# Optimization experiments

Measured on AMD Instinct MI355X. Metric: run time of the kernel, lower is better.

Reference implementation:

```python
import jax, jax.numpy as jnp
from jax import lax
import numpy as np


def setup_inputs() -> dict:
    key = jax.random.key(0)
    k1, k2, k3 = jax.random.split(key, 3)
    B, H, W, C = 8, 128, 128, 128
    F, KS = 128, 3
    x = jax.random.normal(k1, (B, H, W, C), dtype=jnp.float32)
    style = jax.random.normal(k2, (B, C), dtype=jnp.float32)
    kernel = jax.random.normal(k3, (KS, KS, C, F), dtype=jnp.float32) * 0.05
    return {"x": x, "style": style, "kernel": kernel}


def reference(x, style, kernel):
    """StyleGAN2 modulated+demodulated conv via grouped conv (groups=batch).
    x: (B,H,W,C) NHWC, style: (B,C), kernel: (kh,kw,C,F)."""
    B, H, W, C = x.shape
    kh, kw, Cin, F = kernel.shape
    # Modulate: per-sample scale of input channels -> (B, kh, kw, C, F)
    w = kernel[None] * (style[:, None, None, :, None] + 1.0)
    # Demodulate: normalize each output filter over (kh, kw, Cin)
    w = w / jnp.sqrt(jnp.sum(jnp.square(w), axis=(1, 2, 3), keepdims=True) + 1e-8)
    # Grouped conv trick: fold batch into channels, groups = B
    xg = jnp.transpose(x, (0, 3, 1, 2)).reshape(1, B * C, H, W)   # (1, B*C, H, W)
    wg = jnp.transpose(w, (1, 2, 3, 0, 4)).reshape(kh, kw, Cin, B * F)  # HWIO
    y = lax.conv_general_dilated(
        xg, wg, window_strides=(1, 1), padding="SAME",
        dimension_numbers=("NCHW", "HWIO", "NCHW"),
        feature_group_count=B,
    )  # (1, B*F, H, W)
    y = y.reshape(B, F, H, W)
    return jnp.transpose(y, (0, 2, 3, 1))  # NHWC
```

## Files before the change

### kernel.cpp

```cpp
#include <hip/hip_runtime.h>

typedef __attribute__((ext_vector_type(8))) short short8;
typedef __attribute__((ext_vector_type(8))) unsigned short ushort8;
typedef __attribute__((ext_vector_type(4))) float f32x4;

static __device__ __forceinline__ unsigned short f2bf(float f) {
    union { float f; unsigned int u; } a; a.f = f;
    unsigned int u = a.u;
    return (unsigned short)((u + 0x7fffu + ((u >> 16) & 1u)) >> 16);
}

static __device__ __forceinline__ void gll16(const unsigned short* g, unsigned short* l) {
    __builtin_amdgcn_global_load_lds(
        (const __attribute__((address_space(1))) unsigned int*)g,
        (__attribute__((address_space(3))) unsigned int*)l, 16, 0, 0);
}

#define PROW 16640
#define PPLANE 2163200

__global__ void prep1(const float* __restrict__ x,
                      const float* __restrict__ kern,
                      const float* __restrict__ style,
                      float* __restrict__ partial,
                      unsigned short* __restrict__ xbf) {
    const int t = threadIdx.x;
    if (blockIdx.x < 72) {
        const int rs = blockIdx.x % 9;
        const int b  = blockIdx.x / 9;
        __shared__ float sty[128];
        __shared__ float red[256];
        if (t < 128) sty[t] = style[b * 128 + t] + 1.0f;
        __syncthreads();
        const int f = t & 127, half = t >> 7;
        const float* kp = kern + (size_t)rs * 16384 + f;
        float s = 0.0f;
        #pragma unroll 8
        for (int c = half * 64; c < half * 64 + 64; ++c) {
            float w = kp[(size_t)c * 128] * sty[c];
            s += w * w;
        }
        red[t] = s;
        __syncthreads();
        if (t < 128) partial[((size_t)b * 9 + rs) * 128 + t] = red[t] + red[t + 128];
    } else {
        const int id = (blockIdx.x - 72) * 256 + t;
        if (id >= 8 * 130 * 130 * 16) return;
        const int cg = id & 15;
        const int p  = id >> 4;
        const int wp = p % 130;
        const int q  = p / 130;
        const int hp = q % 130;
        const int b  = q / 130;
        ushort8 v = {0, 0, 0, 0, 0, 0, 0, 0};
        if (hp >= 1 && hp <= 128 && wp >= 1 && wp <= 128) {
            const float4* src = (const float4*)(x + (((size_t)b * 128 + (hp - 1)) * 128 + (wp - 1)) * 128 + cg * 8);
            float4 f0 = src[0];
            float4 f1 = src[1];
            v[0] = f2bf(f0.x); v[1] = f2bf(f0.y); v[2] = f2bf(f0.z); v[3] = f2bf(f0.w);
            v[4] = f2bf(f1.x); v[5] = f2bf(f1.y); v[6] = f2bf(f1.z); v[7] = f2bf(f1.w);
        }
        *(ushort8*)(xbf + (size_t)p * 128 + cg * 8) = v;
    }
}

__global__ void prep_wt(const float* __restrict__ kern,
                        const float* __restrict__ style,
                        const float* __restrict__ partial,
                        unsigned short* __restrict__ wt) {
    const int rs = blockIdx.x, b = blockIdx.y;
    const int t  = threadIdx.x;
    __shared__ float sty[128], dm[128];
    __shared__ float ts[32][132];
    if (t < 128) {
        sty[t] = style[b * 128 + t] + 1.0f;
    } else {
        const int f = t - 128;
        float s = 0.0f;
        #pragma unroll
        for (int r = 0; r < 9; ++r) s += partial[((size_t)b * 9 + r) * 128 + f];
        dm[f] = rsqrtf(s + 1e-8f);
    }
    __syncthreads();
    const float* kp = kern + (size_t)rs * 16384;
    unsigned short* wp = wt + ((size_t)b * 9 + rs) * 16384;
    for (int c0 = 0; c0 < 128; c0 += 32) {
        {
            const int fi = (t & 31) * 4;
            const int ci = t >> 5;
            #pragma unroll
            for (int k = 0; k < 4; ++k) {
                const float4 v = *(const float4*)(kp + (size_t)(c0 + ci + 8 * k) * 128 + fi);
                ts[ci + 8 * k][fi + 0] = v.x;
                ts[ci + 8 * k][fi + 1] = v.y;
                ts[ci + 8 * k][fi + 2] = v.z;
                ts[ci + 8 * k][fi + 3] = v.w;
            }
        }
        __syncthreads();
        {
            const int cb = (t & 7) * 4;
            const int f2 = t >> 3;
            #pragma unroll
            for (int k = 0; k < 4; ++k) {
                const int f = f2 + 32 * k;
                ushort4 o;
                o.x = f2bf(ts[cb + 0][f] * sty[c0 + cb + 0] * dm[f]);
                o.y = f2bf(ts[cb + 1][f] * sty[c0 + cb + 1] * dm[f]);
                o.z = f2bf(ts[cb + 2][f] * sty[c0 + cb + 2] * dm[f]);
                o.w = f2bf(ts[cb + 3][f] * sty[c0 + cb + 3] * dm[f]);
                *(ushort4*)(wp + (size_t)f * 128 + c0 + cb) = o;
            }
        }
        __syncthreads();
    }
}

__global__ __launch_bounds__(512, 4) void mdconv7(const unsigned short* __restrict__ xbf,
                                                  const unsigned short* __restrict__ wt,
                                                  float* __restrict__ out) {
    const int lin = blockIdx.x;
    const int b   = lin & 7;
    const int h2  = (lin >> 3) * 2;
    const int tid = threadIdx.x;

    __shared__ unsigned short lsh[2 * 12288];

    const unsigned short* xb  = xbf + (size_t)b * PPLANE;
    const unsigned short* wtb = wt + (size_t)b * 9 * 16384;

    const int so = (tid & 127) * 128 + (tid >> 7) * 8;

    const int lane = tid & 63;
    const int wv   = tid >> 6;
    const int hw   = wv >> 2;
    const int ww   = (wv >> 1) & 1;
    const int fw   = wv & 1;
    const int fl   = lane & 15;
    const int quad = lane >> 4;

    const int ard = hw * 4096 + quad * 1024 + (ww * 64 + fl) * 8;
    const int brd = 8192 + quad * 1024 + (fw * 64 + fl) * 8;

    f32x4 acc[4][4];
    #pragma unroll
    for (int mt = 0; mt < 4; ++mt)
        #pragma unroll
        for (int ft = 0; ft < 4; ++ft)
            acc[mt][ft] = (f32x4){0.f, 0.f, 0.f, 0.f};

#define STAGE(st, nxt) {                                                          \
    const int rs_ = (st) >> 2, kc_ = (st) & 3;                                    \
    const int r_ = rs_ / 3, s_ = rs_ % 3;                                         \
    const unsigned short* ga0 = xb + ((size_t)(h2 + r_) * 130 + s_) * 128 + kc_ * 32; \
    const unsigned short* gb  = wtb + rs_ * 16384 + kc_ * 32;                     \
    unsigned short* la = lsh + (nxt) * 12288;                                     \
    gll16(ga0 + so,        la + tid * 8);                                         \
    gll16(ga0 + PROW + so, la + 4096 + tid * 8);                                  \
    gll16(gb + so,         la + 8192 + tid * 8);                                  \
}

    STAGE(0, 0);
    __syncthreads();

    #pragma unroll
    for (int st = 0; st < 36; ++st) {
        const int cur = st & 1;
        if (st < 35) STAGE(st + 1, cur ^ 1);
        const int ce = cur * 12288;
        short8 bv[4];
        #pragma unroll
        for (int ft = 0; ft < 4; ++ft)
            bv[ft] = *(const short8*)(lsh + ce + brd + ft * 128);
        #pragma unroll
        for (int mt = 0; mt < 4; ++mt) {
            const short8 av = *(const short8*)(lsh + ce + ard + mt * 128);
            #pragma unroll
            for (int ft = 0; ft < 4; ++ft)
                acc[mt][ft] = __builtin_amdgcn_mfma_f32_16x16x32_bf16(av, bv[ft], acc[mt][ft], 0, 0, 0);
        }
        __syncthreads();
    }
#undef STAGE

    float* ob = out + ((size_t)(b * 128 + h2 + hw) * 128) * 128;
    #pragma unroll
    for (int mt = 0; mt < 4; ++mt) {
        #pragma unroll
        for (int reg = 0; reg < 4; ++reg) {
            const int w = ww * 64 + mt * 16 + quad * 4 + reg;
            #pragma unroll
            for (int ft = 0; ft < 4; ++ft)
                ob[(size_t)w * 128 + fw * 64 + ft * 16 + fl] = acc[mt][ft][reg];
        }
    }
}

__global__ void prep_sumsq(const float* __restrict__ kern,
                           const float* __restrict__ style,
                           float* __restrict__ partial) {
    const int rs = blockIdx.x;
    const int b  = blockIdx.y;
    const int t  = threadIdx.x;
    __shared__ float sty[128];
    __shared__ float red[256];
    if (t < 128) sty[t] = style[b * 128 + t] + 1.0f;
    __syncthreads();
    const int f = t & 127, half = t >> 7;
    const float* kp = kern + (size_t)rs * 16384 + f;
    float s = 0.0f;
    #pragma unroll 8
    for (int c = half * 64; c < half * 64 + 64; ++c) {
        float w = kp[(size_t)c * 128] * sty[c];
        s += w * w;
    }
    red[t] = s;
    __syncthreads();
    if (t < 128) partial[((size_t)b * 9 + rs) * 128 + t] = red[t] + red[t + 128];
}

__global__ void mdconv_fb(const float* __restrict__ x,
                          const unsigned short* __restrict__ wt,
                          float* __restrict__ out) {
    const int lin = blockIdx.x;
    const int b   = lin & 7;
    const int sp  = lin >> 3;
    const int h0  = (sp >> 3) * 8;
    const int w0  = (sp & 7) * 16;
    const int tid = threadIdx.x;
    __shared__ unsigned short xs[180 * 138];
    {
        const float* xb = x + (size_t)b * (128 * 128 * 128);
        for (int id = tid; id < 180 * 16; id += 256) {
            int p  = id >> 4;
            int cg = id & 15;
            int pr = p / 18;
            int pc = p - pr * 18;
            int hh = h0 - 1 + pr;
            int ww = w0 - 1 + pc;
            ushort8 v = {0, 0, 0, 0, 0, 0, 0, 0};
            if ((unsigned)hh < 128u && (unsigned)ww < 128u) {
                const float4* src = (const float4*)(xb + ((size_t)(hh * 128 + ww) * 128 + cg * 8));
                float4 f0 = src[0];
                float4 f1 = src[1];
                v[0] = f2bf(f0.x); v[1] = f2bf(f0.y); v[2] = f2bf(f0.z); v[3] = f2bf(f0.w);
                v[4] = f2bf(f1.x); v[5] = f2bf(f1.y); v[6] = f2bf(f1.z); v[7] = f2bf(f1.w);
            }
            *(ushort8*)(xs + p * 138 + cg * 8) = v;
        }
    }
    __syncthreads();
    const int lane = tid & 63;
    const int wave = tid >> 6;
    const int fl   = lane & 15;
    const int quad = lane >> 4;
    const int kq   = quad * 8;
    f32x4 acc[8][2];
    #pragma unroll
    for (int mt = 0; mt < 8; ++mt)
        #pragma unroll
        for (int j = 0; j < 2; ++j)
            acc[mt][j] = (f32x4){0.f, 0.f, 0.f, 0.f};
    const unsigned short* wtb = wt + (size_t)b * (9 * 128 * 128) + (size_t)wave * 4096 + fl * 128 + kq;
    #pragma unroll
    for (int rs = 0; rs < 9; ++rs) {
        const int r = rs / 3, s = rs % 3;
        #pragma unroll
        for (int kc = 0; kc < 4; ++kc) {
            const int k0 = kc * 32 + kq;
            short8 a[8];
            #pragma unroll
            for (int mt = 0; mt < 8; ++mt)
                a[mt] = *(const short8*)(xs + ((mt + r) * 18 + fl + s) * 138 + k0);
            #pragma unroll
            for (int j = 0; j < 2; ++j) {
                short8 bf = *(const short8*)(wtb + rs * 16384 + j * 2048 + kc * 32);
                #pragma unroll
                for (int mt = 0; mt < 8; ++mt)
                    acc[mt][j] = __builtin_amdgcn_mfma_f32_16x16x32_bf16(a[mt], bf, acc[mt][j], 0, 0, 0);
            }
        }
    }
    float* ob = out + ((size_t)(b * 128 + h0) * 128 + w0) * 128;
    #pragma unroll
    for (int mt = 0; mt < 8; ++mt)
        #pragma unroll
        for (int j = 0; j < 2; ++j) {
            const int f = (wave * 2 + j) * 16 + fl;
            #pragma unroll
            for (int reg = 0; reg < 4; ++reg)
                ob[((size_t)(mt * 128 + quad * 4 + reg)) * 128 + f] = acc[mt][j][reg];
        }
}

extern "C" void kernel_launch(void* const* d_in, const int* in_sizes, int n_in,
                              void* d_out, int out_size, void* d_ws, size_t ws_size,
                              hipStream_t stream) {
    const float* x     = (const float*)d_in[0];
    const float* style = (const float*)d_in[1];
    const float* kern  = (const float*)d_in[2];
    float* out = (float*)d_out;

    const size_t XBF_BYTES = (size_t)8 * 130 * 130 * 128 * 2;
    const size_t WT_BYTES  = (size_t)8 * 9 * 128 * 128 * 2;
    const size_t NEED      = XBF_BYTES + WT_BYTES + 36864;

    if (ws_size >= NEED) {
        unsigned short* xbf = (unsigned short*)d_ws;
        unsigned short* wt  = (unsigned short*)((char*)d_ws + XBF_BYTES);
        float* partial      = (float*)((char*)d_ws + XBF_BYTES + WT_BYTES);
        prep1<<<dim3(72 + 8450), dim3(256), 0, stream>>>(x, kern, style, partial, xbf);
        prep_wt<<<dim3(9, 8), dim3(256), 0, stream>>>(kern, style, partial, wt);
        mdconv7<<<dim3(512), dim3(512), 0, stream>>>(xbf, wt, out);
    } else {
        unsigned short* wt = (unsigned short*)d_ws;
        float* partial     = (float*)((char*)d_ws + WT_BYTES);
        prep_sumsq<<<dim3(9, 8), dim3(256), 0, stream>>>(kern, style, partial);
        prep_wt<<<dim3(9, 8), dim3(256), 0, stream>>>(kern, style, partial, wt);
        mdconv_fb<<<dim3(1024), dim3(256), 0, stream>>>(x, wt, out);
    }
}
```

Before: 183.2 us.

## Shrink conv tile to one output row per block with 256 threads

Each block of the main conv kernel now computes one output row instead of two, with 4 waves instead of 8, and the grid doubles to 1024 blocks. LDS per stage shrinks from 24 KB to 16 KB because only one input row is staged alongside the weight slice. This aims to raise occupancy and spread work across more blocks on the CUs. The cost is lower weight reuse, since each weight slice is loaded once per row instead of once per pair of rows, which roughly doubles weight traffic.

```diff
diff --git a/kernel.cpp b/kernel.cpp
--- a/kernel.cpp
+++ b/kernel.cpp
@@ -116,15 +116,15 @@
     }
 }
 
-__global__ __launch_bounds__(512, 4) void mdconv7(const unsigned short* __restrict__ xbf,
+__global__ __launch_bounds__(256, 4) void mdconv8(const unsigned short* __restrict__ xbf,
                                                   const unsigned short* __restrict__ wt,
                                                   float* __restrict__ out) {
     const int lin = blockIdx.x;
     const int b   = lin & 7;
-    const int h2  = (lin >> 3) * 2;
+    const int h   = lin >> 3;
     const int tid = threadIdx.x;
 
-    __shared__ unsigned short lsh[2 * 12288];
+    __shared__ unsigned short lsh[2 * 8192];
 
     const unsigned short* xb  = xbf + (size_t)b * PPLANE;
     const unsigned short* wtb = wt + (size_t)b * 9 * 16384;
@@ -133,14 +133,12 @@
 
     const int lane = tid & 63;
     const int wv   = tid >> 6;
-    const int hw   = wv >> 2;
-    const int ww   = (wv >> 1) & 1;
-    const int fw   = wv & 1;
     const int fl   = lane & 15;
     const int quad = lane >> 4;
-
-    const int ard = hw * 4096 + quad * 1024 + (ww * 64 + fl) * 8;
-    const int brd = 8192 + quad * 1024 + (fw * 64 + fl) * 8;
+    const int wrb  = (wv >> 1) * 64;
+    const int fcb  = (wv & 1) * 64;
+    const int ab_rd = quad * 1024 + (wrb + fl) * 8;
+    const int bb_rd = 4096 + quad * 1024 + (fcb + fl) * 8;
 
     f32x4 acc[4][4];
     #pragma unroll
@@ -152,12 +150,13 @@
 #define STAGE(st, nxt) {                                                          \
     const int rs_ = (st) >> 2, kc_ = (st) & 3;                                    \
     const int r_ = rs_ / 3, s_ = rs_ % 3;                                         \
-    const unsigned short* ga0 = xb + ((size_t)(h2 + r_) * 130 + s_) * 128 + kc_ * 32; \
-    const unsigned short* gb  = wtb + rs_ * 16384 + kc_ * 32;                     \
-    unsigned short* la = lsh + (nxt) * 12288;                                     \
-    gll16(ga0 + so,        la + tid * 8);                                         \
-    gll16(ga0 + PROW + so, la + 4096 + tid * 8);                                  \
-    gll16(gb + so,         la + 8192 + tid * 8);                                  \
+    const unsigned short* ga = xb + ((size_t)(h + r_) * 130 + s_) * 128 + kc_ * 32; \
+    const unsigned short* gb = wtb + rs_ * 16384 + kc_ * 32;                      \
+    unsigned short* la = lsh + (nxt) * 8192;                                      \
+    gll16(ga + so,      la + tid * 8);                                            \
+    gll16(ga + so + 16, la + 2048 + tid * 8);                                     \
+    gll16(gb + so,      la + 4096 + tid * 8);                                     \
+    gll16(gb + so + 16, la + 6144 + tid * 8);                                     \
 }
 
     STAGE(0, 0);
@@ -167,14 +166,14 @@
     for (int st = 0; st < 36; ++st) {
         const int cur = st & 1;
         if (st < 35) STAGE(st + 1, cur ^ 1);
-        const int ce = cur * 12288;
+        const int ce = cur * 8192;
         short8 bv[4];
         #pragma unroll
         for (int ft = 0; ft < 4; ++ft)
-            bv[ft] = *(const short8*)(lsh + ce + brd + ft * 128);
+            bv[ft] = *(const short8*)(lsh + ce + bb_rd + ft * 128);
         #pragma unroll
         for (int mt = 0; mt < 4; ++mt) {
-            const short8 av = *(const short8*)(lsh + ce + ard + mt * 128);
+            const short8 av = *(const short8*)(lsh + ce + ab_rd + mt * 128);
             #pragma unroll
             for (int ft = 0; ft < 4; ++ft)
                 acc[mt][ft] = __builtin_amdgcn_mfma_f32_16x16x32_bf16(av, bv[ft], acc[mt][ft], 0, 0, 0);
@@ -183,15 +182,15 @@
     }
 #undef STAGE
 
-    float* ob = out + ((size_t)(b * 128 + h2 + hw) * 128) * 128;
+    float* ob = out + ((size_t)(b * 128 + h) * 128) * 128;
     #pragma unroll
     for (int mt = 0; mt < 4; ++mt) {
         #pragma unroll
         for (int reg = 0; reg < 4; ++reg) {
-            const int w = ww * 64 + mt * 16 + quad * 4 + reg;
+            const int w = wrb + mt * 16 + quad * 4 + reg;
             #pragma unroll
             for (int ft = 0; ft < 4; ++ft)
-                ob[(size_t)w * 128 + fw * 64 + ft * 16 + fl] = acc[mt][ft][reg];
+                ob[(size_t)w * 128 + fcb + ft * 16 + fl] = acc[mt][ft][reg];
         }
     }
 }
@@ -311,7 +310,7 @@
         float* partial      = (float*)((char*)d_ws + XBF_BYTES + WT_BYTES);
         prep1<<<dim3(72 + 8450), dim3(256), 0, stream>>>(x, kern, style, partial, xbf);
         prep_wt<<<dim3(9, 8), dim3(256), 0, stream>>>(kern, style, partial, wt);
-        mdconv7<<<dim3(512), dim3(512), 0, stream>>>(xbf, wt, out);
+        mdconv8<<<dim3(1024), dim3(256), 0, stream>>>(xbf, wt, out);
     } else {
         unsigned short* wt = (unsigned short*)d_ws;
         float* partial     = (float*)((char*)d_ws + WT_BYTES);
```

Result: slower. 203.0 us (+10.8%).
